# Kernel tuning notes

Measured on AMD Instinct MI355X. Metric: run time of the kernel, lower is better.

## Reference

```python
import jax, jax.numpy as jnp
import numpy as np

H = 1024   # hidden_size
NH = 16    # num heads
HD = H // NH


def setup_inputs() -> dict:
    key = jax.random.key(0)
    ks = jax.random.split(key, 6)
    B, S = 4, 2048
    hidden_states = jax.random.normal(ks[0], (B, S, H), dtype=jnp.float32)
    attention_mask = jnp.zeros((B, S), dtype=jnp.float32)  # additive mask
    scale = 1.0 / np.sqrt(H)
    Wq = jax.random.normal(ks[1], (H, H), dtype=jnp.float32) * scale
    Wk = jax.random.normal(ks[2], (H, H), dtype=jnp.float32) * scale
    Wv = jax.random.normal(ks[3], (H, H), dtype=jnp.float32) * scale
    Wo = jax.random.normal(ks[4], (H, H), dtype=jnp.float32) * scale
    return {"hidden_states": hidden_states, "attention_mask": attention_mask,
            "Wq": Wq, "Wk": Wk, "Wv": Wv, "Wo": Wo}


def reference(hidden_states, attention_mask, Wq, Wk, Wv, Wo):
    B, S, _ = hidden_states.shape
    scaling = HD ** -0.5
    # nn.Linear: y = x @ W.T ; split heads -> [B, NH, S, HD]
    def heads(x, W):
        return (x @ W.T).reshape(B, S, NH, HD).transpose(0, 2, 1, 3)
    q = heads(hidden_states, Wq)
    k = heads(hidden_states, Wk)
    v = heads(hidden_states, Wv)
    scores = jnp.einsum('bhqd,bhkd->bhqk', q, k) * scaling
    scores = scores + attention_mask[:, None, None, :]
    weights = jax.nn.softmax(scores, axis=-1)
    attn = jnp.einsum('bhqk,bhkd->bhqd', weights, v)
    attn = attn.transpose(0, 2, 1, 3).reshape(B, S, H)
    return attn @ Wo.T
```

## Files before the change

kernel.cpp:

```cpp
#include <hip/hip_runtime.h>
#include <hip/hip_bf16.h>

#define B_ 4
#define S_ 2048
#define H_ 1024
#define NH_ 16
#define HD_ 64
#define QSCALE 0.1803368801111204f

typedef __bf16 bf16_t;
typedef bf16_t bf16x8 __attribute__((ext_vector_type(8)));
typedef bf16_t bf16x4 __attribute__((ext_vector_type(4)));
typedef bf16_t bf16x2t __attribute__((ext_vector_type(2)));
typedef float f32x4 __attribute__((ext_vector_type(4)));
typedef unsigned u32x2 __attribute__((ext_vector_type(2)));
typedef unsigned u32x4 __attribute__((ext_vector_type(4)));

__device__ __forceinline__ f32x4 mfma16(bf16x8 a, bf16x8 b, f32x4 c) {
  return __builtin_amdgcn_mfma_f32_16x16x32_bf16(a, b, c, 0, 0, 0);
}

extern "C" __device__ float __ocml_native_exp2_f32(float);
__device__ __forceinline__ float fast_exp2(float x) {
  return __ocml_native_exp2_f32(x);
}

__device__ __forceinline__ void gll16(const bf16_t* g, bf16_t* l) {
  __builtin_amdgcn_global_load_lds(
      (const __attribute__((address_space(1))) void*)g,
      (__attribute__((address_space(3))) void*)l, 16, 0, 0);
}

__device__ __forceinline__ bf16x8 frag64(const bf16_t* lds, int row,
                                         int kchunk) {
  return *(const bf16x8*)((const char*)lds + row * 128 +
                          ((kchunk ^ (row & 7)) << 4));
}

__device__ __forceinline__ void stage128(const bf16_t* gbase, int gstride,
                                         bf16_t* lds, int w, int lane) {
#pragma unroll
  for (int j = 0; j < 4; ++j) {
    int seg = w * 4 + j;
    int row = seg * 8 + (lane >> 3);
    int chunk = (lane & 7) ^ (row & 7);
    gll16(gbase + (size_t)row * gstride + chunk * 8, lds + seg * 512);
  }
}

__global__ __launch_bounds__(256) void cvt_all(
    const float* __restrict__ X, const float* __restrict__ Wq,
    const float* __restrict__ Wk, const float* __restrict__ Wv,
    const float* __restrict__ Wo, const float* __restrict__ mask,
    bf16_t* __restrict__ Xb, bf16_t* __restrict__ Wqb,
    bf16_t* __restrict__ Wkb, bf16_t* __restrict__ Wvb,
    bf16_t* __restrict__ Wob, float* __restrict__ maskl) {
  size_t i = ((size_t)blockIdx.x * 256 + threadIdx.x) * 4;
  const float* src;
  bf16_t* dst;
  size_t off;
  float scale = 1.0f;
  if (i < 8388608) {
    src = X; dst = Xb; off = i;
  } else {
    size_t j = i - 8388608;
    if (j >= 4194304) {
      size_t mo = j - 4194304;
      float4 mv = *(const float4*)(mask + mo);
      const float LOG2E = 1.4426950408889634f;
      float4 ml = {mv.x * LOG2E, mv.y * LOG2E, mv.z * LOG2E, mv.w * LOG2E};
      *(float4*)(maskl + mo) = ml;
      return;
    }
    int w = (int)(j >> 20);
    off = j & 1048575;
    switch (w) {
      case 0: src = Wq; dst = Wqb; scale = QSCALE; break;
      case 1: src = Wk; dst = Wkb; break;
      case 2: src = Wv; dst = Wvb; break;
      default: src = Wo; dst = Wob; break;
    }
  }
  float4 v = *(const float4*)(src + off);
  bf16x4 o = {(bf16_t)(v.x * scale), (bf16_t)(v.y * scale),
              (bf16_t)(v.z * scale), (bf16_t)(v.w * scale)};
  *(bf16x4*)(dst + off) = o;
}

__device__ __forceinline__ void gemm_core(const bf16_t* __restrict__ A,
                                          const bf16_t* __restrict__ Bw,
                                          int Mb, int Nb, bf16_t* As,
                                          bf16_t* Bs, f32x4 (*acc)[4], int w,
                                          int lane, int quad, int l15, int wm,
                                          int wn) {
  for (int kb = 0; kb < 16; ++kb) {
    stage128(A + (size_t)Mb * 1024 + kb * 64, 1024, As, w, lane);
    stage128(Bw + (size_t)Nb * 1024 + kb * 64, 1024, Bs, w, lane);
    __syncthreads();
#pragma unroll
    for (int kt = 0; kt < 2; ++kt) {
      bf16x8 af[4], bfr[4];
#pragma unroll
      for (int i = 0; i < 4; ++i) {
        af[i] = frag64(As, wm * 64 + i * 16 + l15, kt * 4 + quad);
        bfr[i] = frag64(Bs, wn * 64 + i * 16 + l15, kt * 4 + quad);
      }
      __builtin_amdgcn_s_setprio(1);
#pragma unroll
      for (int mt = 0; mt < 4; ++mt)
#pragma unroll
        for (int nt = 0; nt < 4; ++nt)
          acc[mt][nt] = mfma16(af[mt], bfr[nt], acc[mt][nt]);
      __builtin_amdgcn_s_setprio(0);
    }
    __syncthreads();
  }
}

__global__ __launch_bounds__(256) void gemm_qkv(
    const bf16_t* __restrict__ Xb, const bf16_t* __restrict__ Wqb,
    const bf16_t* __restrict__ Wkb, const bf16_t* __restrict__ Wvb,
    bf16_t* __restrict__ q_ws, bf16_t* __restrict__ k_ws,
    bf16_t* __restrict__ vt_ws) {
  __shared__ __align__(16) bf16_t As[8192];
  __shared__ __align__(16) bf16_t Bs[8192];
  int w = threadIdx.x >> 6, lane = threadIdx.x & 63;
  int quad = lane >> 4, l15 = lane & 15;
  int wm = w >> 1, wn = w & 1;
  int z = blockIdx.z;
  const bf16_t* A = (z == 2) ? Wvb : Xb;
  const bf16_t* Bw = (z == 0) ? Wqb : ((z == 1) ? Wkb : Xb);
  int Mb = (z == 2) ? blockIdx.y * 128 : blockIdx.x * 128;
  int Nb = (z == 2) ? blockIdx.x * 128 : blockIdx.y * 128;
  f32x4 acc[4][4] = {};
  gemm_core(A, Bw, Mb, Nb, As, Bs, acc, w, lane, quad, l15, wm, wn);
  if (z != 2) {
    bf16_t* O = (z == 0) ? q_ws : k_ws;
#pragma unroll
    for (int mt = 0; mt < 4; ++mt) {
      int m0t = Mb + wm * 64 + mt * 16;
#pragma unroll
      for (int nt = 0; nt < 4; ++nt) {
        int n0t = Nb + wn * 64 + nt * 16;
        int h = n0t >> 6, d = (n0t & 63) + l15;
#pragma unroll
        for (int r = 0; r < 4; ++r) {
          int tok = m0t + quad * 4 + r;
          int b = tok >> 11, s = tok & 2047;
          O[(((size_t)b * NH_ + h) * S_ + s) * HD_ + d] = (bf16_t)acc[mt][nt][r];
        }
      }
    }
  } else {
#pragma unroll
    for (int mt = 0; mt < 4; ++mt) {
      int m0t = Mb + wm * 64 + mt * 16;
#pragma unroll
      for (int nt = 0; nt < 4; ++nt) {
        int n0t = Nb + wn * 64 + nt * 16;
#pragma unroll
        for (int r = 0; r < 4; ++r) {
          int dg = m0t + quad * 4 + r;
          int hh = dg >> 6, d = dg & 63;
          int tok = n0t + l15;
          int b = tok >> 11, s = tok & 2047;
          vt_ws[((size_t)(b * NH_ + hh) * HD_ + d) * S_ + s] =
              (bf16_t)acc[mt][nt][r];
        }
      }
    }
  }
}

__global__ __launch_bounds__(256) void gemm_out(
    const bf16_t* __restrict__ A, const bf16_t* __restrict__ Bw,
    float* __restrict__ out) {
  __shared__ __align__(16) bf16_t As[8192];
  __shared__ __align__(16) bf16_t Bs[8192];
  int w = threadIdx.x >> 6, lane = threadIdx.x & 63;
  int quad = lane >> 4, l15 = lane & 15;
  int wm = w >> 1, wn = w & 1;
  int Mb = blockIdx.x * 128, Nb = blockIdx.y * 128;
  f32x4 acc[4][4] = {};
  gemm_core(A, Bw, Mb, Nb, As, Bs, acc, w, lane, quad, l15, wm, wn);
#pragma unroll
  for (int mt = 0; mt < 4; ++mt) {
    int m0t = Mb + wm * 64 + mt * 16;
#pragma unroll
    for (int nt = 0; nt < 4; ++nt) {
      int n0t = Nb + wn * 64 + nt * 16;
#pragma unroll
      for (int r = 0; r < 4; ++r)
        out[(size_t)(m0t + quad * 4 + r) * 1024 + n0t + l15] = acc[mt][nt][r];
    }
  }
}

__global__ __launch_bounds__(256, 3) void attn_fused(
    const bf16_t* __restrict__ Q, const bf16_t* __restrict__ K,
    const bf16_t* __restrict__ Vt, const float* __restrict__ maskl,
    bf16_t* __restrict__ Oa) {
  __shared__ __align__(16) bf16_t Ks[2][4096];
  __shared__ __align__(16) bf16_t Vs[2][4096];
  int w = threadIdx.x >> 6, lane = threadIdx.x & 63;
  int quad = lane >> 4, l15 = lane & 15;
  int bh = blockIdx.x;
  int b = bh >> 4, h = bh & 15;
  int q0 = blockIdx.y * 128 + w * 32;
  const bf16_t* Qh = Q + (size_t)bh * (S_ * HD_);
  const bf16_t* Kh = K + (size_t)bh * (S_ * HD_);
  const bf16_t* Vh = Vt + (size_t)bh * (HD_ * S_);
  const float* mb = maskl + b * S_;
  const bf16_t one_b = (bf16_t)1.0f;
  bf16x8 ones = {one_b, one_b, one_b, one_b, one_b, one_b, one_b, one_b};

  int srow[2], schunk[2], lseg[2];
#pragma unroll
  for (int j = 0; j < 2; ++j) {
    int seg = w * 2 + j;
    srow[j] = seg * 8 + (lane >> 3);
    schunk[j] = (lane & 7) ^ (srow[j] & 7);
    lseg[j] = seg * 512;
  }

  bf16x8 qf[2][2];
#pragma unroll
  for (int nt = 0; nt < 2; ++nt)
#pragma unroll
    for (int kt = 0; kt < 2; ++kt)
      qf[nt][kt] = *(const bf16x8*)(Qh + (size_t)(q0 + nt * 16 + l15) * HD_ +
                                    kt * 32 + quad * 8);

  f32x4 oc[4][2] = {};
  f32x4 lc[2] = {};

#pragma unroll
  for (int j = 0; j < 2; ++j) {
    gll16(Kh + (size_t)srow[j] * HD_ + schunk[j] * 8, &Ks[0][0] + lseg[j]);
    gll16(Vh + (size_t)srow[j] * S_ + schunk[j] * 8, &Vs[0][0] + lseg[j]);
  }
  f32x4 mreg[4];
#pragma unroll
  for (int mt = 0; mt < 4; ++mt)
    mreg[mt] = *(const f32x4*)(mb + mt * 16 + quad * 4);
  __syncthreads();

  for (int c = 0; c < 32; ++c) {
    int cur = c & 1;
    if (c + 1 < 32) {
      const bf16_t* Kc = Kh + (size_t)(c + 1) * 64 * HD_;
      const bf16_t* Vc = Vh + (size_t)(c + 1) * 64;
#pragma unroll
      for (int j = 0; j < 2; ++j) {
        gll16(Kc + (size_t)srow[j] * HD_ + schunk[j] * 8,
              &Ks[cur ^ 1][0] + lseg[j]);
        gll16(Vc + (size_t)srow[j] * S_ + schunk[j] * 8,
              &Vs[cur ^ 1][0] + lseg[j]);
      }
    }
    f32x4 sc[4][2];
#pragma unroll
    for (int mt = 0; mt < 4; ++mt)
#pragma unroll
      for (int nt = 0; nt < 2; ++nt) sc[mt][nt] = mreg[mt];
    if (c + 1 < 32) {
#pragma unroll
      for (int mt = 0; mt < 4; ++mt)
        mreg[mt] = *(const f32x4*)(mb + (c + 1) * 64 + mt * 16 + quad * 4);
    }
#pragma unroll
    for (int kt = 0; kt < 2; ++kt) {
      bf16x8 kf[4];
#pragma unroll
      for (int mt = 0; mt < 4; ++mt)
        kf[mt] = frag64(Ks[cur], mt * 16 + l15, kt * 4 + quad);
#pragma unroll
      for (int mt = 0; mt < 4; ++mt)
#pragma unroll
        for (int nt = 0; nt < 2; ++nt)
          sc[mt][nt] = mfma16(kf[mt], qf[nt][kt], sc[mt][nt]);
    }
#pragma unroll
    for (int kt = 0; kt < 2; ++kt) {
      unsigned pk[2][2][2];
#pragma unroll
      for (int mi = 0; mi < 2; ++mi) {
        int mt = kt * 2 + mi;
#pragma unroll
        for (int nt = 0; nt < 2; ++nt) {
          f32x4 p;
#pragma unroll
          for (int r = 0; r < 4; ++r) p[r] = fast_exp2(sc[mt][nt][r]);
          bf16x2t h0 = {(bf16_t)p[0], (bf16_t)p[1]};
          bf16x2t h1 = {(bf16_t)p[2], (bf16_t)p[3]};
          pk[mi][nt][0] = __builtin_bit_cast(unsigned, h0);
          pk[mi][nt][1] = __builtin_bit_cast(unsigned, h1);
        }
      }
      bf16x8 pf[2];
#pragma unroll
      for (int nt = 0; nt < 2; ++nt) {
        u32x2 a0 = __builtin_amdgcn_permlane32_swap(pk[0][nt][0],
                                                    pk[1][nt][0],
                                                    false, false);
        u32x2 b0 = __builtin_amdgcn_permlane16_swap(a0.x, a0.y, false, false);
        u32x2 a1 = __builtin_amdgcn_permlane32_swap(pk[0][nt][1],
                                                    pk[1][nt][1],
                                                    false, false);
        u32x2 b1 = __builtin_amdgcn_permlane16_swap(a1.x, a1.y, false, false);
        u32x4 pu = {b0.x, b1.x, b0.y, b1.y};
        pf[nt] = __builtin_bit_cast(bf16x8, pu);
      }
      lc[0] = mfma16(ones, pf[0], lc[0]);
      lc[1] = mfma16(ones, pf[1], lc[1]);
#pragma unroll
      for (int dt = 0; dt < 4; ++dt) {
        bf16x8 vf = frag64(Vs[cur], dt * 16 + l15, kt * 4 + quad);
#pragma unroll
        for (int nt = 0; nt < 2; ++nt)
          oc[dt][nt] = mfma16(vf, pf[nt], oc[dt][nt]);
      }
    }
    __syncthreads();
  }
  float inv[2] = {1.0f / lc[0][0], 1.0f / lc[1][0]};
#pragma unroll
  for (int dt = 0; dt < 4; ++dt)
#pragma unroll
    for (int nt = 0; nt < 2; ++nt) {
      bf16x4 o4;
#pragma unroll
      for (int r = 0; r < 4; ++r) o4[r] = (bf16_t)(oc[dt][nt][r] * inv[nt]);
      size_t tok = (size_t)b * S_ + q0 + nt * 16 + l15;
      *(bf16x4*)(Oa + tok * H_ + h * HD_ + dt * 16 + quad * 4) = o4;
    }
}

extern "C" void kernel_launch(void* const* d_in, const int* in_sizes, int n_in,
                              void* d_out, int out_size, void* d_ws,
                              size_t ws_size, hipStream_t stream) {
  const float* hs   = (const float*)d_in[0];
  const float* mask = (const float*)d_in[1];
  const float* Wq   = (const float*)d_in[2];
  const float* Wk   = (const float*)d_in[3];
  const float* Wv   = (const float*)d_in[4];
  const float* Wo   = (const float*)d_in[5];
  float* out = (float*)d_out;

  char* p = (char*)d_ws;
  bf16_t* Xb  = (bf16_t*)p; p += (size_t)8192 * 1024 * 2;
  bf16_t* Wqb = (bf16_t*)p; p += (size_t)1024 * 1024 * 2;
  bf16_t* Wkb = (bf16_t*)p; p += (size_t)1024 * 1024 * 2;
  bf16_t* Wvb = (bf16_t*)p; p += (size_t)1024 * 1024 * 2;
  bf16_t* Wob = (bf16_t*)p; p += (size_t)1024 * 1024 * 2;
  bf16_t* q_ws  = (bf16_t*)p; p += (size_t)8192 * 1024 * 2;
  bf16_t* k_ws  = (bf16_t*)p; p += (size_t)8192 * 1024 * 2;
  bf16_t* vt_ws = (bf16_t*)p; p += (size_t)8192 * 1024 * 2;
  float* maskl = (float*)p; p += (size_t)B_ * S_ * 4;
  bf16_t* attn_b = Xb;

  cvt_all<<<12296, 256, 0, stream>>>(hs, Wq, Wk, Wv, Wo, mask, Xb, Wqb, Wkb,
                                     Wvb, Wob, maskl);
  gemm_qkv<<<dim3(64, 8, 3), 256, 0, stream>>>(Xb, Wqb, Wkb, Wvb, q_ws, k_ws,
                                               vt_ws);
  attn_fused<<<dim3(64, 16), 256, 0, stream>>>(q_ws, k_ws, vt_ws, maskl,
                                               attn_b);
  gemm_out<<<dim3(64, 8), 256, 0, stream>>>(attn_b, Wob, out);
}
```

Before: 246.8 us.

## Widen attention blocks to 8 waves with 128-key stages and MFMA priority hints

Each attention block now runs 512 threads covering 256 queries, and every pipeline stage loads 128 keys into two 64-key sub-buffers. This halves the number of K/V tile loads across blocks and the number of block-wide barriers per key pass. It also wraps the MFMA sections in s_setprio so matrix work is favoured over other waves' exp and permute code. In exchange the block uses twice the LDS (64 KB), and larger blocks with fewer resident per CU may reduce latency hiding.

```diff
diff --git a/kernel.cpp b/kernel.cpp
--- a/kernel.cpp
+++ b/kernel.cpp
@@ -196,17 +196,17 @@
   }
 }
 
-__global__ __launch_bounds__(256, 3) void attn_fused(
+__global__ __launch_bounds__(512, 2) void attn_fused(
     const bf16_t* __restrict__ Q, const bf16_t* __restrict__ K,
     const bf16_t* __restrict__ Vt, const float* __restrict__ maskl,
     bf16_t* __restrict__ Oa) {
-  __shared__ __align__(16) bf16_t Ks[2][4096];
-  __shared__ __align__(16) bf16_t Vs[2][4096];
+  __shared__ __align__(16) bf16_t Ks[2][2][4096];
+  __shared__ __align__(16) bf16_t Vs[2][2][4096];
   int w = threadIdx.x >> 6, lane = threadIdx.x & 63;
   int quad = lane >> 4, l15 = lane & 15;
   int bh = blockIdx.x;
   int b = bh >> 4, h = bh & 15;
-  int q0 = blockIdx.y * 128 + w * 32;
+  int q0 = blockIdx.y * 256 + w * 32;
   const bf16_t* Qh = Q + (size_t)bh * (S_ * HD_);
   const bf16_t* Kh = K + (size_t)bh * (S_ * HD_);
   const bf16_t* Vh = Vt + (size_t)bh * (HD_ * S_);
@@ -214,13 +214,15 @@
   const bf16_t one_b = (bf16_t)1.0f;
   bf16x8 ones = {one_b, one_b, one_b, one_b, one_b, one_b, one_b, one_b};
 
-  int srow[2], schunk[2], lseg[2];
+  int sub[2], row[2], chk[2], segb[2];
 #pragma unroll
   for (int j = 0; j < 2; ++j) {
     int seg = w * 2 + j;
-    srow[j] = seg * 8 + (lane >> 3);
-    schunk[j] = (lane & 7) ^ (srow[j] & 7);
-    lseg[j] = seg * 512;
+    sub[j] = seg >> 3;
+    int rb = seg & 7;
+    row[j] = rb * 8 + (lane >> 3);
+    chk[j] = (lane & 7) ^ (row[j] & 7);
+    segb[j] = rb * 512;
   }
 
   bf16x8 qf[2][2];
@@ -236,8 +238,10 @@
 
 #pragma unroll
   for (int j = 0; j < 2; ++j) {
-    gll16(Kh + (size_t)srow[j] * HD_ + schunk[j] * 8, &Ks[0][0] + lseg[j]);
-    gll16(Vh + (size_t)srow[j] * S_ + schunk[j] * 8, &Vs[0][0] + lseg[j]);
+    gll16(Kh + (size_t)(sub[j] * 64 + row[j]) * HD_ + chk[j] * 8,
+          &Ks[0][sub[j]][segb[j]]);
+    gll16(Vh + (size_t)row[j] * S_ + sub[j] * 64 + chk[j] * 8,
+          &Vs[0][sub[j]][segb[j]]);
   }
   f32x4 mreg[4];
 #pragma unroll
@@ -245,80 +249,90 @@
     mreg[mt] = *(const f32x4*)(mb + mt * 16 + quad * 4);
   __syncthreads();
 
-  for (int c = 0; c < 32; ++c) {
-    int cur = c & 1;
-    if (c + 1 < 32) {
-      const bf16_t* Kc = Kh + (size_t)(c + 1) * 64 * HD_;
-      const bf16_t* Vc = Vh + (size_t)(c + 1) * 64;
+  for (int p = 0; p < 16; ++p) {
+    int buf = p & 1;
+    if (p + 1 < 16) {
+      const bf16_t* Kp = Kh + (size_t)(p + 1) * 128 * HD_;
+      const bf16_t* Vp = Vh + (size_t)(p + 1) * 128;
 #pragma unroll
       for (int j = 0; j < 2; ++j) {
-        gll16(Kc + (size_t)srow[j] * HD_ + schunk[j] * 8,
-              &Ks[cur ^ 1][0] + lseg[j]);
-        gll16(Vc + (size_t)srow[j] * S_ + schunk[j] * 8,
-              &Vs[cur ^ 1][0] + lseg[j]);
-      }
-    }
-    f32x4 sc[4][2];
-#pragma unroll
-    for (int mt = 0; mt < 4; ++mt)
-#pragma unroll
-      for (int nt = 0; nt < 2; ++nt) sc[mt][nt] = mreg[mt];
-    if (c + 1 < 32) {
+        gll16(Kp + (size_t)(sub[j] * 64 + row[j]) * HD_ + chk[j] * 8,
+              &Ks[buf ^ 1][sub[j]][segb[j]]);
+        gll16(Vp + (size_t)row[j] * S_ + sub[j] * 64 + chk[j] * 8,
+              &Vs[buf ^ 1][sub[j]][segb[j]]);
+      }
+    }
+#pragma unroll
+    for (int s = 0; s < 2; ++s) {
+      int c = p * 2 + s;
+      f32x4 sc[4][2];
 #pragma unroll
       for (int mt = 0; mt < 4; ++mt)
-        mreg[mt] = *(const f32x4*)(mb + (c + 1) * 64 + mt * 16 + quad * 4);
-    }
-#pragma unroll
-    for (int kt = 0; kt < 2; ++kt) {
-      bf16x8 kf[4];
-#pragma unroll
-      for (int mt = 0; mt < 4; ++mt)
-        kf[mt] = frag64(Ks[cur], mt * 16 + l15, kt * 4 + quad);
-#pragma unroll
-      for (int mt = 0; mt < 4; ++mt)
-#pragma unroll
-        for (int nt = 0; nt < 2; ++nt)
-          sc[mt][nt] = mfma16(kf[mt], qf[nt][kt], sc[mt][nt]);
-    }
-#pragma unroll
-    for (int kt = 0; kt < 2; ++kt) {
-      unsigned pk[2][2][2];
-#pragma unroll
-      for (int mi = 0; mi < 2; ++mi) {
-        int mt = kt * 2 + mi;
+#pragma unroll
+        for (int nt = 0; nt < 2; ++nt) sc[mt][nt] = mreg[mt];
+      if (c + 1 < 32) {
+#pragma unroll
+        for (int mt = 0; mt < 4; ++mt)
+          mreg[mt] = *(const f32x4*)(mb + (c + 1) * 64 + mt * 16 + quad * 4);
+      }
+#pragma unroll
+      for (int kt = 0; kt < 2; ++kt) {
+        bf16x8 kf[4];
+#pragma unroll
+        for (int mt = 0; mt < 4; ++mt)
+          kf[mt] = frag64(Ks[buf][s], mt * 16 + l15, kt * 4 + quad);
+        __builtin_amdgcn_s_setprio(1);
+#pragma unroll
+        for (int mt = 0; mt < 4; ++mt)
+#pragma unroll
+          for (int nt = 0; nt < 2; ++nt)
+            sc[mt][nt] = mfma16(kf[mt], qf[nt][kt], sc[mt][nt]);
+        __builtin_amdgcn_s_setprio(0);
+      }
+#pragma unroll
+      for (int kt = 0; kt < 2; ++kt) {
+        unsigned pk[2][2][2];
+#pragma unroll
+        for (int mi = 0; mi < 2; ++mi) {
+          int mt = kt * 2 + mi;
+#pragma unroll
+          for (int nt = 0; nt < 2; ++nt) {
+            f32x4 pv;
+#pragma unroll
+            for (int r = 0; r < 4; ++r) pv[r] = fast_exp2(sc[mt][nt][r]);
+            bf16x2t h0 = {(bf16_t)pv[0], (bf16_t)pv[1]};
+            bf16x2t h1 = {(bf16_t)pv[2], (bf16_t)pv[3]};
+            pk[mi][nt][0] = __builtin_bit_cast(unsigned, h0);
+            pk[mi][nt][1] = __builtin_bit_cast(unsigned, h1);
+          }
+        }
+        bf16x8 pf[2];
 #pragma unroll
         for (int nt = 0; nt < 2; ++nt) {
-          f32x4 p;
-#pragma unroll
-          for (int r = 0; r < 4; ++r) p[r] = fast_exp2(sc[mt][nt][r]);
-          bf16x2t h0 = {(bf16_t)p[0], (bf16_t)p[1]};
-          bf16x2t h1 = {(bf16_t)p[2], (bf16_t)p[3]};
-          pk[mi][nt][0] = __builtin_bit_cast(unsigned, h0);
-          pk[mi][nt][1] = __builtin_bit_cast(unsigned, h1);
-        }
-      }
-      bf16x8 pf[2];
-#pragma unroll
-      for (int nt = 0; nt < 2; ++nt) {
-        u32x2 a0 = __builtin_amdgcn_permlane32_swap(pk[0][nt][0],
-                                                    pk[1][nt][0],
-                                                    false, false);
-        u32x2 b0 = __builtin_amdgcn_permlane16_swap(a0.x, a0.y, false, false);
-        u32x2 a1 = __builtin_amdgcn_permlane32_swap(pk[0][nt][1],
-                                                    pk[1][nt][1],
-                                                    false, false);
-        u32x2 b1 = __builtin_amdgcn_permlane16_swap(a1.x, a1.y, false, false);
-        u32x4 pu = {b0.x, b1.x, b0.y, b1.y};
-        pf[nt] = __builtin_bit_cast(bf16x8, pu);
-      }
-      lc[0] = mfma16(ones, pf[0], lc[0]);
-      lc[1] = mfma16(ones, pf[1], lc[1]);
-#pragma unroll
-      for (int dt = 0; dt < 4; ++dt) {
-        bf16x8 vf = frag64(Vs[cur], dt * 16 + l15, kt * 4 + quad);
-#pragma unroll
-        for (int nt = 0; nt < 2; ++nt)
-          oc[dt][nt] = mfma16(vf, pf[nt], oc[dt][nt]);
+          u32x2 a0 = __builtin_amdgcn_permlane32_swap(pk[0][nt][0],
+                                                      pk[1][nt][0],
+                                                      false, false);
+          u32x2 b0 = __builtin_amdgcn_permlane16_swap(a0.x, a0.y, false,
+                                                      false);
+          u32x2 a1 = __builtin_amdgcn_permlane32_swap(pk[0][nt][1],
+                                                      pk[1][nt][1],
+                                                      false, false);
+          u32x2 b1 = __builtin_amdgcn_permlane16_swap(a1.x, a1.y, false,
+                                                      false);
+          u32x4 pu = {b0.x, b1.x, b0.y, b1.y};
+          pf[nt] = __builtin_bit_cast(bf16x8, pu);
+        }
+        __builtin_amdgcn_s_setprio(1);
+        lc[0] = mfma16(ones, pf[0], lc[0]);
+        lc[1] = mfma16(ones, pf[1], lc[1]);
+#pragma unroll
+        for (int dt = 0; dt < 4; ++dt) {
+          bf16x8 vf = frag64(Vs[buf][s], dt * 16 + l15, kt * 4 + quad);
+#pragma unroll
+          for (int nt = 0; nt < 2; ++nt)
+            oc[dt][nt] = mfma16(vf, pf[nt], oc[dt][nt]);
+        }
+        __builtin_amdgcn_s_setprio(0);
       }
     }
     __syncthreads();
@@ -363,7 +377,7 @@
                                      Wvb, Wob, maskl);
   gemm_qkv<<<dim3(64, 8, 3), 256, 0, stream>>>(Xb, Wqb, Wkb, Wvb, q_ws, k_ws,
                                                vt_ws);
-  attn_fused<<<dim3(64, 16), 256, 0, stream>>>(q_ws, k_ws, vt_ws, maskl,
-                                               attn_b);
+  attn_fused<<<dim3(64, 8), 512, 0, stream>>>(q_ws, k_ws, vt_ws, maskl,
+                                              attn_b);
   gemm_out<<<dim3(64, 8), 256, 0, stream>>>(attn_b, Wob, out);
 }
```

Result: slower. 260.8 us (+5.7%).
